# Kernel tuning notes

Hardware: AMD Instinct MI355X
Metric: run time of the kernel (lower is better)

## Reference

```python
import jax, jax.numpy as jnp
import numpy as np

B, C, H, W, P = 16, 512, 64, 64, 32


def setup_inputs() -> dict:
    key = jax.random.key(0)
    k1, k2, k3 = jax.random.split(key, 3)
    inputs = jax.random.normal(k1, (B, C, H, W), dtype=jnp.float32)
    weight = jax.random.uniform(k2, (P, C, 1, 1), dtype=jnp.float32)
    smooth_factor = jax.random.normal(k3, (P,), dtype=jnp.float32)
    return {"inputs": inputs, "weight": weight, "smooth_factor": smooth_factor}


def reference(inputs, weight, smooth_factor):
    b, c, h, w = inputs.shape
    p = weight.shape[0]
    n = h * w
    centers = weight.reshape(p, c)                      # [P,C]
    x = inputs.reshape(b, c, n)                         # [B,C,N]

    # distance-based logits: 2<c,x> - |x|^2 - |c|^2, clamped at 0
    cx = jnp.einsum('pc,bcn->bpn', centers, x)          # [B,P,N]
    x_sq = jnp.sum(x * x, axis=1, keepdims=True)        # [B,1,N]
    c_sq = jnp.sum(centers * centers, axis=1)[None, :, None]  # [1,P,1]
    beta = jax.nn.sigmoid(smooth_factor)                # [P]
    logits = jnp.minimum(2.0 * cx - x_sq - c_sq, 0.0) / beta[None, :, None]
    assign = jax.nn.softmax(logits, axis=1)             # [B,P,N]

    # assignment-weighted pooling
    qx = jnp.einsum('bpn,bcn->bpc', assign, x)          # [B,P,C]
    sum_ass = jnp.clip(jnp.sum(assign, axis=2, keepdims=True), 1e-5)  # [B,P,1]
    sigma = jnp.sqrt(beta / 2.0)                        # [P]
    out = (qx / sum_ass - centers[None, :, :]) / sigma[None, :, None]

    # L2-normalize over channel dim (torch F.normalize, eps=1e-12)
    norm = jnp.sqrt(jnp.sum(out * out, axis=2, keepdims=True))
    outputs = out / jnp.maximum(norm, 1e-12)
    outputs_t = jnp.transpose(outputs, (0, 2, 1))       # [B,C,P]
    assign_map = assign.reshape(b, p, h, w)             # [B,P,H,W]
    return outputs_t, assign_map
```

## Files before the change

### kernel.cpp

```cpp
#include <hip/hip_runtime.h>

constexpr int BB = 16;
constexpr int CC = 512;
constexpr int PP = 32;
constexpr int NN = 4096;
constexpr int TN = 128;

using f32x4 = __attribute__((ext_vector_type(4))) float;
using bf16x8 = __attribute__((ext_vector_type(8))) short;
typedef unsigned int uint;

__device__ __forceinline__ ushort f2bf(float f) {
  unsigned u = __builtin_bit_cast(unsigned, f);
  u += 0x7FFFu + ((u >> 16) & 1u);
  return (ushort)(u >> 16);
}

__device__ __forceinline__ uint packbf(float f) {
  uint u = __builtin_bit_cast(uint, f);
  uint hi = (u + (0x7FFFu + ((u >> 16) & 1u))) >> 16;
  float hif = __builtin_bit_cast(float, hi << 16);
  float lof = f - hif;
  uint ul = __builtin_bit_cast(uint, lof);
  uint lo = (ul + (0x7FFFu + ((ul >> 16) & 1u))) >> 16;
  return (lo << 16) | hi;
}

struct BfPair { bf16x8 hi, lo; };

__device__ __forceinline__ BfPair unpack8(const uint* __restrict__ row, int co) {
  uint4 a = *(const uint4*)(row + co);
  uint4 b = *(const uint4*)(row + co + 4);
  union { bf16x8 v; uint d[4]; } H, L;
  H.d[0] = (a.x & 0xffffu) | (a.y << 16); L.d[0] = (a.x >> 16) | (a.y & 0xffff0000u);
  H.d[1] = (a.z & 0xffffu) | (a.w << 16); L.d[1] = (a.z >> 16) | (a.w & 0xffff0000u);
  H.d[2] = (b.x & 0xffffu) | (b.y << 16); L.d[2] = (b.x >> 16) | (b.y & 0xffff0000u);
  H.d[3] = (b.z & 0xffffu) | (b.w << 16); L.d[3] = (b.z >> 16) | (b.w & 0xffff0000u);
  return {H.v, L.v};
}

__global__ __launch_bounds__(64) void prep_kernel(
    const float* __restrict__ w, const float* __restrict__ sf,
    float* __restrict__ beta, float* __restrict__ rbeta,
    float* __restrict__ csq) {
  int p = blockIdx.x;
  int t = threadIdx.x;
  float s = 0.f;
  for (int i = t; i < CC; i += 64) {
    float v = w[p * CC + i];
    s = fmaf(v, v, s);
  }
#pragma unroll
  for (int off = 32; off; off >>= 1) s += __shfl_down(s, off);
  if (t == 0) {
    csq[p] = s;
    float e = __expf(-sf[p]);
    rbeta[p] = 1.f + e;
    beta[p] = 1.f / (1.f + e);
  }
}

__global__ __launch_bounds__(256, 3) void fused_kernel(
    const float* __restrict__ x, const float* __restrict__ w,
    const float* __restrict__ rbeta_, const float* __restrict__ csq_,
    float* __restrict__ assign_out, float* __restrict__ sum_ass,
    float* __restrict__ qx) {
  __shared__ uint xpk[128][68];
  __shared__ uint cpk[32][68];
  __shared__ float xsqw[4][4][32];
  __shared__ float xsqf[128];
  ushort(*xt)[136] = (ushort(*)[136]) & xpk[0][0];
  ushort(*abf)[136] = (ushort(*)[136]) & cpk[0][0];

  int tid = threadIdx.x;
  int wv = tid >> 6, lane = tid & 63;
  int l15 = lane & 15, lg = lane >> 4;
  int b = blockIdx.x >> 5;
  int n0 = (blockIdx.x & 31) * TN;

  int c_s = tid >> 2;
  int q = tid & 3;
  int p_s = tid >> 3;
  int cq8 = (tid & 7) << 3;

  const float* xb = x + (size_t)b * CC * NN + n0 + q * 32;
  const float* wb = w + (size_t)p_s * CC + cq8;

  f32x4 acc[2][2];
#pragma unroll
  for (int i = 0; i < 2; ++i)
#pragma unroll
    for (int j = 0; j < 2; ++j) acc[i][j] = {0.f, 0.f, 0.f, 0.f};
  float sq[32];
#pragma unroll
  for (int i = 0; i < 32; ++i) sq[i] = 0.f;

  float4 xr[8], wr0, wr1;
#pragma unroll
  for (int i = 0; i < 8; ++i)
    xr[i] = *(const float4*)&xb[(size_t)c_s * NN + i * 4];
  wr0 = *(const float4*)&wb[0];
  wr1 = *(const float4*)&wb[4];
#pragma unroll
  for (int i = 0; i < 8; ++i) {
    float4 v = xr[i];
    sq[4 * i + 0] = fmaf(v.x, v.x, sq[4 * i + 0]);
    sq[4 * i + 1] = fmaf(v.y, v.y, sq[4 * i + 1]);
    sq[4 * i + 2] = fmaf(v.z, v.z, sq[4 * i + 2]);
    sq[4 * i + 3] = fmaf(v.w, v.w, sq[4 * i + 3]);
    int nr = q * 32 + i * 4;
    xpk[nr + 0][c_s] = packbf(v.x);
    xpk[nr + 1][c_s] = packbf(v.y);
    xpk[nr + 2][c_s] = packbf(v.z);
    xpk[nr + 3][c_s] = packbf(v.w);
  }
  {
    uint4 u0 = {packbf(wr0.x), packbf(wr0.y), packbf(wr0.z), packbf(wr0.w)};
    uint4 u1 = {packbf(wr1.x), packbf(wr1.y), packbf(wr1.z), packbf(wr1.w)};
    *(uint4*)&cpk[p_s][cq8] = u0;
    *(uint4*)&cpk[p_s][cq8 + 4] = u1;
  }
  __syncthreads();

  for (int c0 = 0; c0 < CC; c0 += 64) {
    bool more = (c0 + 64 < CC);
    if (more) {
#pragma unroll
      for (int i = 0; i < 8; ++i)
        xr[i] = *(const float4*)&xb[(size_t)(c0 + 64 + c_s) * NN + i * 4];
      wr0 = *(const float4*)&wb[c0 + 64];
      wr1 = *(const float4*)&wb[c0 + 64 + 4];
    }
#pragma unroll
    for (int ks = 0; ks < 2; ++ks) {
      int co = ks * 32 + lg * 8;
      BfPair A0 = unpack8(&cpk[l15][0], co);
      BfPair A1 = unpack8(&cpk[l15 + 16][0], co);
      BfPair B0 = unpack8(&xpk[wv * 32 + l15][0], co);
      BfPair B1 = unpack8(&xpk[wv * 32 + 16 + l15][0], co);
      acc[0][0] = __builtin_amdgcn_mfma_f32_16x16x32_bf16(A0.hi, B0.hi, acc[0][0], 0, 0, 0);
      acc[0][1] = __builtin_amdgcn_mfma_f32_16x16x32_bf16(A0.hi, B1.hi, acc[0][1], 0, 0, 0);
      acc[1][0] = __builtin_amdgcn_mfma_f32_16x16x32_bf16(A1.hi, B0.hi, acc[1][0], 0, 0, 0);
      acc[1][1] = __builtin_amdgcn_mfma_f32_16x16x32_bf16(A1.hi, B1.hi, acc[1][1], 0, 0, 0);
      acc[0][0] = __builtin_amdgcn_mfma_f32_16x16x32_bf16(A0.hi, B0.lo, acc[0][0], 0, 0, 0);
      acc[0][1] = __builtin_amdgcn_mfma_f32_16x16x32_bf16(A0.hi, B1.lo, acc[0][1], 0, 0, 0);
      acc[1][0] = __builtin_amdgcn_mfma_f32_16x16x32_bf16(A1.hi, B0.lo, acc[1][0], 0, 0, 0);
      acc[1][1] = __builtin_amdgcn_mfma_f32_16x16x32_bf16(A1.hi, B1.lo, acc[1][1], 0, 0, 0);
      acc[0][0] = __builtin_amdgcn_mfma_f32_16x16x32_bf16(A0.lo, B0.hi, acc[0][0], 0, 0, 0);
      acc[0][1] = __builtin_amdgcn_mfma_f32_16x16x32_bf16(A0.lo, B1.hi, acc[0][1], 0, 0, 0);
      acc[1][0] = __builtin_amdgcn_mfma_f32_16x16x32_bf16(A1.lo, B0.hi, acc[1][0], 0, 0, 0);
      acc[1][1] = __builtin_amdgcn_mfma_f32_16x16x32_bf16(A1.lo, B1.hi, acc[1][1], 0, 0, 0);
    }
    if (more) {
      __syncthreads();
#pragma unroll
      for (int i = 0; i < 8; ++i) {
        float4 v = xr[i];
        sq[4 * i + 0] = fmaf(v.x, v.x, sq[4 * i + 0]);
        sq[4 * i + 1] = fmaf(v.y, v.y, sq[4 * i + 1]);
        sq[4 * i + 2] = fmaf(v.z, v.z, sq[4 * i + 2]);
        sq[4 * i + 3] = fmaf(v.w, v.w, sq[4 * i + 3]);
        int nr = q * 32 + i * 4;
        xpk[nr + 0][c_s] = packbf(v.x);
        xpk[nr + 1][c_s] = packbf(v.y);
        xpk[nr + 2][c_s] = packbf(v.z);
        xpk[nr + 3][c_s] = packbf(v.w);
      }
      uint4 u0 = {packbf(wr0.x), packbf(wr0.y), packbf(wr0.z), packbf(wr0.w)};
      uint4 u1 = {packbf(wr1.x), packbf(wr1.y), packbf(wr1.z), packbf(wr1.w)};
      *(uint4*)&cpk[p_s][cq8] = u0;
      *(uint4*)&cpk[p_s][cq8 + 4] = u1;
      __syncthreads();
    }
  }

#pragma unroll
  for (int i = 0; i < 32; ++i) {
    sq[i] += __shfl_xor(sq[i], 4);
    sq[i] += __shfl_xor(sq[i], 8);
    sq[i] += __shfl_xor(sq[i], 16);
    sq[i] += __shfl_xor(sq[i], 32);
  }
  if ((lane >> 2) == 0) {
#pragma unroll
    for (int i = 0; i < 32; ++i) xsqw[wv][lane & 3][i] = sq[i];
  }
  __syncthreads();
  if (tid < 128)
    xsqf[tid] = xsqw[0][tid >> 5][tid & 31] + xsqw[1][tid >> 5][tid & 31] +
                xsqw[2][tid >> 5][tid & 31] + xsqw[3][tid >> 5][tid & 31];
  __syncthreads();

  float xsqn0 = xsqf[wv * 32 + l15];
  float xsqn1 = xsqf[wv * 32 + 16 + l15];

  float csqv[2][4], rbv[2][4];
#pragma unroll
  for (int pf = 0; pf < 2; ++pf)
#pragma unroll
    for (int i = 0; i < 4; ++i) {
      int p = pf * 16 + lg * 4 + i;
      csqv[pf][i] = csq_[p];
      rbv[pf][i] = rbeta_[p];
    }

  float L[2][2][4];
  float m0 = -3.4e38f, m1 = -3.4e38f;
#pragma unroll
  for (int pf = 0; pf < 2; ++pf)
#pragma unroll
    for (int i = 0; i < 4; ++i) {
      float l0 = fminf(2.f * acc[pf][0][i] - xsqn0 - csqv[pf][i], 0.f) * rbv[pf][i];
      float l1 = fminf(2.f * acc[pf][1][i] - xsqn1 - csqv[pf][i], 0.f) * rbv[pf][i];
      L[pf][0][i] = l0; L[pf][1][i] = l1;
      m0 = fmaxf(m0, l0); m1 = fmaxf(m1, l1);
    }
  m0 = fmaxf(m0, __shfl_xor(m0, 16)); m0 = fmaxf(m0, __shfl_xor(m0, 32));
  m1 = fmaxf(m1, __shfl_xor(m1, 16)); m1 = fmaxf(m1, __shfl_xor(m1, 32));
  float s0 = 0.f, s1 = 0.f;
#pragma unroll
  for (int pf = 0; pf < 2; ++pf)
#pragma unroll
    for (int i = 0; i < 4; ++i) {
      float e0 = __expf(L[pf][0][i] - m0);
      float e1 = __expf(L[pf][1][i] - m1);
      L[pf][0][i] = e0; L[pf][1][i] = e1;
      s0 += e0; s1 += e1;
    }
  s0 += __shfl_xor(s0, 16); s0 += __shfl_xor(s0, 32);
  s1 += __shfl_xor(s1, 16); s1 += __shfl_xor(s1, 32);
  float inv0 = 1.f / s0, inv1 = 1.f / s1;

  float* aoB = assign_out + (size_t)b * PP * NN + n0 + wv * 32 + l15;
#pragma unroll
  for (int pf = 0; pf < 2; ++pf)
#pragma unroll
    for (int i = 0; i < 4; ++i) {
      int p = pf * 16 + lg * 4 + i;
      float a0 = L[pf][0][i] * inv0;
      float a1 = L[pf][1][i] * inv1;
      aoB[(size_t)p * NN] = a0;
      aoB[(size_t)p * NN + 16] = a1;
      abf[p][wv * 32 + l15] = f2bf(a0);
      abf[p][wv * 32 + 16 + l15] = f2bf(a1);
      float v = a0 + a1;
      v += __shfl_xor(v, 1); v += __shfl_xor(v, 2);
      v += __shfl_xor(v, 4); v += __shfl_xor(v, 8);
      if (l15 == 0) atomicAdd(&sum_ass[b * PP + p], v);
    }

  int c_s2 = tid >> 1;
  int nh2 = (tid & 1) << 6;
  const float* xg = x + (size_t)b * CC * NN + n0;

  for (int ch = 0; ch < 4; ++ch) {
    __syncthreads();
#pragma unroll
    for (int h = 0; h < 2; ++h) {
      float4 v[8];
#pragma unroll
      for (int i = 0; i < 8; ++i)
        v[i] = *(const float4*)&xg[(size_t)(ch * 128 + c_s2) * NN + nh2 + h * 32 + i * 4];
#pragma unroll
      for (int i = 0; i < 8; ++i) {
        ushort4 u;
        u.x = f2bf(v[i].x); u.y = f2bf(v[i].y);
        u.z = f2bf(v[i].z); u.w = f2bf(v[i].w);
        *(ushort4*)&xt[c_s2][nh2 + h * 32 + i * 4] = u;
      }
    }
    __syncthreads();

    f32x4 q2[2][2];
#pragma unroll
    for (int pf = 0; pf < 2; ++pf)
#pragma unroll
      for (int cf = 0; cf < 2; ++cf) q2[pf][cf] = {0.f, 0.f, 0.f, 0.f};
#pragma unroll
    for (int ks = 0; ks < 4; ++ks) {
      int ko = ks * 32 + lg * 8;
      bf16x8 A0 = *(const bf16x8*)&abf[l15][ko];
      bf16x8 A1 = *(const bf16x8*)&abf[l15 + 16][ko];
#pragma unroll
      for (int cf = 0; cf < 2; ++cf) {
        bf16x8 Bv = *(const bf16x8*)&xt[wv * 32 + cf * 16 + l15][ko];
        q2[0][cf] = __builtin_amdgcn_mfma_f32_16x16x32_bf16(A0, Bv, q2[0][cf], 0, 0, 0);
        q2[1][cf] = __builtin_amdgcn_mfma_f32_16x16x32_bf16(A1, Bv, q2[1][cf], 0, 0, 0);
      }
    }
#pragma unroll
    for (int pf = 0; pf < 2; ++pf)
#pragma unroll
      for (int cf = 0; cf < 2; ++cf)
#pragma unroll
        for (int i = 0; i < 4; ++i) {
          int p = pf * 16 + lg * 4 + i;
          int c = ch * 128 + wv * 32 + cf * 16 + l15;
          atomicAdd(&qx[((size_t)b * PP + p) * CC + c], q2[pf][cf][i]);
        }
  }
}

__global__ __launch_bounds__(256) void finalize_kernel(
    const float* __restrict__ qx, const float* __restrict__ w,
    const float* __restrict__ beta, const float* __restrict__ sum_ass,
    float* __restrict__ out_t) {
  int b = blockIdx.x >> 5;
  int p = blockIdx.x & 31;
  int tid = threadIdx.x;
  int wave = tid >> 6, lane = tid & 63;

  float inv_sa = 1.f / fmaxf(sum_ass[b * PP + p], 1e-5f);
  float rsig = rsqrtf(0.5f * beta[p]);

  int c0 = tid, c1 = tid + 256;
  const float* qrow = qx + ((size_t)b * PP + p) * CC;
  const float* wrow = w + (size_t)p * CC;
  float t0 = (qrow[c0] * inv_sa - wrow[c0]) * rsig;
  float t1 = (qrow[c1] * inv_sa - wrow[c1]) * rsig;

  float nr = t0 * t0 + t1 * t1;
#pragma unroll
  for (int off = 32; off; off >>= 1) nr += __shfl_down(nr, off);
  __shared__ float red[4];
  if (lane == 0) red[wave] = nr;
  __syncthreads();
  float norm2 = red[0] + red[1] + red[2] + red[3];
  float scale = 1.f / fmaxf(sqrtf(norm2), 1e-12f);

  float* ob = out_t + (size_t)b * CC * PP + p;
  ob[(size_t)c0 * PP] = t0 * scale;
  ob[(size_t)c1 * PP] = t1 * scale;
}

extern "C" void kernel_launch(void* const* d_in, const int* in_sizes, int n_in,
                              void* d_out, int out_size, void* d_ws,
                              size_t ws_size, hipStream_t stream) {
  const float* x = (const float*)d_in[0];
  const float* w = (const float*)d_in[1];
  const float* sf = (const float*)d_in[2];

  float* out_t = (float*)d_out;
  float* assign = out_t + (size_t)BB * CC * PP;

  float* ws = (float*)d_ws;
  float* beta = ws;
  float* rbeta = ws + 32;
  float* csq = ws + 64;
  float* sum_ass = ws + 96;
  float* qx = ws + 608;

  hipMemsetAsync(sum_ass, 0, (512 + (size_t)BB * PP * CC) * sizeof(float),
                 stream);
  prep_kernel<<<PP, 64, 0, stream>>>(w, sf, beta, rbeta, csq);
  fused_kernel<<<BB * 32, 256, 0, stream>>>(x, w, rbeta, csq, assign,
                                            sum_ass, qx);
  finalize_kernel<<<BB * PP, 256, 0, stream>>>(qx, w, beta, sum_ass, out_t);
}
```

Baseline: 95.37 us.

## Halve spatial tile to double grid, split qx atomics, fold memset into prep

```diff
diff --git a/kernel.cpp b/kernel.cpp
--- a/kernel.cpp
+++ b/kernel.cpp
@@ -4,7 +4,7 @@
 constexpr int CC = 512;
 constexpr int PP = 32;
 constexpr int NN = 4096;
-constexpr int TN = 128;
+constexpr int TN = 64;
 
 using f32x4 = __attribute__((ext_vector_type(4))) float;
 using bf16x8 = __attribute__((ext_vector_type(8))) short;
@@ -42,73 +42,78 @@
 __global__ __launch_bounds__(64) void prep_kernel(
     const float* __restrict__ w, const float* __restrict__ sf,
     float* __restrict__ beta, float* __restrict__ rbeta,
-    float* __restrict__ csq) {
-  int p = blockIdx.x;
+    float* __restrict__ csq, float* __restrict__ zbuf) {
   int t = threadIdx.x;
-  float s = 0.f;
-  for (int i = t; i < CC; i += 64) {
-    float v = w[p * CC + i];
-    s = fmaf(v, v, s);
-  }
-#pragma unroll
-  for (int off = 32; off; off >>= 1) s += __shfl_down(s, off);
-  if (t == 0) {
-    csq[p] = s;
-    float e = __expf(-sf[p]);
-    rbeta[p] = 1.f + e;
-    beta[p] = 1.f / (1.f + e);
-  }
-}
-
-__global__ __launch_bounds__(256, 3) void fused_kernel(
+  float4* z4 = (float4*)zbuf;
+  for (int i = blockIdx.x * 64 + t; i < 131200; i += 256 * 64)
+    z4[i] = make_float4(0.f, 0.f, 0.f, 0.f);
+  if (blockIdx.x < PP) {
+    int p = blockIdx.x;
+    float s = 0.f;
+    for (int i = t; i < CC; i += 64) {
+      float v = w[p * CC + i];
+      s = fmaf(v, v, s);
+    }
+#pragma unroll
+    for (int off = 32; off; off >>= 1) s += __shfl_down(s, off);
+    if (t == 0) {
+      csq[p] = s;
+      float e = __expf(-sf[p]);
+      rbeta[p] = 1.f + e;
+      beta[p] = 1.f / (1.f + e);
+    }
+  }
+}
+
+__global__ __launch_bounds__(256, 4) void fused_kernel(
     const float* __restrict__ x, const float* __restrict__ w,
     const float* __restrict__ rbeta_, const float* __restrict__ csq_,
     float* __restrict__ assign_out, float* __restrict__ sum_ass,
-    float* __restrict__ qx) {
-  __shared__ uint xpk[128][68];
-  __shared__ uint cpk[32][68];
-  __shared__ float xsqw[4][4][32];
-  __shared__ float xsqf[128];
-  ushort(*xt)[136] = (ushort(*)[136]) & xpk[0][0];
-  ushort(*abf)[136] = (ushort(*)[136]) & cpk[0][0];
+    float* __restrict__ qx2) {
+  __shared__ uint shbuf[6528];
+  __shared__ ushort abf[PP][72];
+  __shared__ float xsqw[4][4][16];
+  __shared__ float xsqf[TN];
+
+  uint(*xpk)[68] = (uint(*)[68])shbuf;
+  uint(*cpk)[68] = (uint(*)[68])(shbuf + 64 * 68);
+  ushort(*xt)[72] = (ushort(*)[72])shbuf;
 
   int tid = threadIdx.x;
   int wv = tid >> 6, lane = tid & 63;
   int l15 = lane & 15, lg = lane >> 4;
-  int b = blockIdx.x >> 5;
-  int n0 = (blockIdx.x & 31) * TN;
+  int b = blockIdx.x >> 6;
+  int n0 = (blockIdx.x & 63) * TN;
 
   int c_s = tid >> 2;
-  int q = tid & 3;
+  int nw = (tid & 3) << 4;
   int p_s = tid >> 3;
   int cq8 = (tid & 7) << 3;
 
-  const float* xb = x + (size_t)b * CC * NN + n0 + q * 32;
+  const float* xb = x + (size_t)b * CC * NN + n0 + nw;
   const float* wb = w + (size_t)p_s * CC + cq8;
 
-  f32x4 acc[2][2];
-#pragma unroll
-  for (int i = 0; i < 2; ++i)
-#pragma unroll
-    for (int j = 0; j < 2; ++j) acc[i][j] = {0.f, 0.f, 0.f, 0.f};
-  float sq[32];
-#pragma unroll
-  for (int i = 0; i < 32; ++i) sq[i] = 0.f;
-
-  float4 xr[8], wr0, wr1;
-#pragma unroll
-  for (int i = 0; i < 8; ++i)
+  f32x4 acc[2];
+  acc[0] = {0.f, 0.f, 0.f, 0.f};
+  acc[1] = {0.f, 0.f, 0.f, 0.f};
+  float sq[16];
+#pragma unroll
+  for (int i = 0; i < 16; ++i) sq[i] = 0.f;
+
+  float4 xr[4], wr0, wr1;
+#pragma unroll
+  for (int i = 0; i < 4; ++i)
     xr[i] = *(const float4*)&xb[(size_t)c_s * NN + i * 4];
   wr0 = *(const float4*)&wb[0];
   wr1 = *(const float4*)&wb[4];
 #pragma unroll
-  for (int i = 0; i < 8; ++i) {
+  for (int i = 0; i < 4; ++i) {
     float4 v = xr[i];
     sq[4 * i + 0] = fmaf(v.x, v.x, sq[4 * i + 0]);
     sq[4 * i + 1] = fmaf(v.y, v.y, sq[4 * i + 1]);
     sq[4 * i + 2] = fmaf(v.z, v.z, sq[4 * i + 2]);
     sq[4 * i + 3] = fmaf(v.w, v.w, sq[4 * i + 3]);
-    int nr = q * 32 + i * 4;
+    int nr = nw + i * 4;
     xpk[nr + 0][c_s] = packbf(v.x);
     xpk[nr + 1][c_s] = packbf(v.y);
     xpk[nr + 2][c_s] = packbf(v.z);
@@ -126,7 +131,7 @@
     bool more = (c0 + 64 < CC);
     if (more) {
 #pragma unroll
-      for (int i = 0; i < 8; ++i)
+      for (int i = 0; i < 4; ++i)
         xr[i] = *(const float4*)&xb[(size_t)(c0 + 64 + c_s) * NN + i * 4];
       wr0 = *(const float4*)&wb[c0 + 64];
       wr1 = *(const float4*)&wb[c0 + 64 + 4];
@@ -136,31 +141,24 @@
       int co = ks * 32 + lg * 8;
       BfPair A0 = unpack8(&cpk[l15][0], co);
       BfPair A1 = unpack8(&cpk[l15 + 16][0], co);
-      BfPair B0 = unpack8(&xpk[wv * 32 + l15][0], co);
-      BfPair B1 = unpack8(&xpk[wv * 32 + 16 + l15][0], co);
-      acc[0][0] = __builtin_amdgcn_mfma_f32_16x16x32_bf16(A0.hi, B0.hi, acc[0][0], 0, 0, 0);
-      acc[0][1] = __builtin_amdgcn_mfma_f32_16x16x32_bf16(A0.hi, B1.hi, acc[0][1], 0, 0, 0);
-      acc[1][0] = __builtin_amdgcn_mfma_f32_16x16x32_bf16(A1.hi, B0.hi, acc[1][0], 0, 0, 0);
-      acc[1][1] = __builtin_amdgcn_mfma_f32_16x16x32_bf16(A1.hi, B1.hi, acc[1][1], 0, 0, 0);
-      acc[0][0] = __builtin_amdgcn_mfma_f32_16x16x32_bf16(A0.hi, B0.lo, acc[0][0], 0, 0, 0);
-      acc[0][1] = __builtin_amdgcn_mfma_f32_16x16x32_bf16(A0.hi, B1.lo, acc[0][1], 0, 0, 0);
-      acc[1][0] = __builtin_amdgcn_mfma_f32_16x16x32_bf16(A1.hi, B0.lo, acc[1][0], 0, 0, 0);
-      acc[1][1] = __builtin_amdgcn_mfma_f32_16x16x32_bf16(A1.hi, B1.lo, acc[1][1], 0, 0, 0);
-      acc[0][0] = __builtin_amdgcn_mfma_f32_16x16x32_bf16(A0.lo, B0.hi, acc[0][0], 0, 0, 0);
-      acc[0][1] = __builtin_amdgcn_mfma_f32_16x16x32_bf16(A0.lo, B1.hi, acc[0][1], 0, 0, 0);
-      acc[1][0] = __builtin_amdgcn_mfma_f32_16x16x32_bf16(A1.lo, B0.hi, acc[1][0], 0, 0, 0);
-      acc[1][1] = __builtin_amdgcn_mfma_f32_16x16x32_bf16(A1.lo, B1.hi, acc[1][1], 0, 0, 0);
+      BfPair B0 = unpack8(&xpk[wv * 16 + l15][0], co);
+      acc[0] = __builtin_amdgcn_mfma_f32_16x16x32_bf16(A0.hi, B0.hi, acc[0], 0, 0, 0);
+      acc[1] = __builtin_amdgcn_mfma_f32_16x16x32_bf16(A1.hi, B0.hi, acc[1], 0, 0, 0);
+      acc[0] = __builtin_amdgcn_mfma_f32_16x16x32_bf16(A0.hi, B0.lo, acc[0], 0, 0, 0);
+      acc[1] = __builtin_amdgcn_mfma_f32_16x16x32_bf16(A1.hi, B0.lo, acc[1], 0, 0, 0);
+      acc[0] = __builtin_amdgcn_mfma_f32_16x16x32_bf16(A0.lo, B0.hi, acc[0], 0, 0, 0);
+      acc[1] = __builtin_amdgcn_mfma_f32_16x16x32_bf16(A1.lo, B0.hi, acc[1], 0, 0, 0);
     }
     if (more) {
       __syncthreads();
 #pragma unroll
-      for (int i = 0; i < 8; ++i) {
+      for (int i = 0; i < 4; ++i) {
         float4 v = xr[i];
         sq[4 * i + 0] = fmaf(v.x, v.x, sq[4 * i + 0]);
         sq[4 * i + 1] = fmaf(v.y, v.y, sq[4 * i + 1]);
         sq[4 * i + 2] = fmaf(v.z, v.z, sq[4 * i + 2]);
         sq[4 * i + 3] = fmaf(v.w, v.w, sq[4 * i + 3]);
-        int nr = q * 32 + i * 4;
+        int nr = nw + i * 4;
         xpk[nr + 0][c_s] = packbf(v.x);
         xpk[nr + 1][c_s] = packbf(v.y);
         xpk[nr + 2][c_s] = packbf(v.z);
@@ -175,98 +173,84 @@
   }
 
 #pragma unroll
-  for (int i = 0; i < 32; ++i) {
+  for (int i = 0; i < 16; ++i) {
     sq[i] += __shfl_xor(sq[i], 4);
     sq[i] += __shfl_xor(sq[i], 8);
     sq[i] += __shfl_xor(sq[i], 16);
     sq[i] += __shfl_xor(sq[i], 32);
   }
-  if ((lane >> 2) == 0) {
-#pragma unroll
-    for (int i = 0; i < 32; ++i) xsqw[wv][lane & 3][i] = sq[i];
+  if (lane < 4) {
+#pragma unroll
+    for (int i = 0; i < 16; ++i) xsqw[wv][lane][i] = sq[i];
   }
   __syncthreads();
-  if (tid < 128)
-    xsqf[tid] = xsqw[0][tid >> 5][tid & 31] + xsqw[1][tid >> 5][tid & 31] +
-                xsqw[2][tid >> 5][tid & 31] + xsqw[3][tid >> 5][tid & 31];
+  if (tid < TN)
+    xsqf[tid] = xsqw[0][tid >> 4][tid & 15] + xsqw[1][tid >> 4][tid & 15] +
+                xsqw[2][tid >> 4][tid & 15] + xsqw[3][tid >> 4][tid & 15];
   __syncthreads();
 
-  float xsqn0 = xsqf[wv * 32 + l15];
-  float xsqn1 = xsqf[wv * 32 + 16 + l15];
-
-  float csqv[2][4], rbv[2][4];
+  float xsqn = xsqf[wv * 16 + l15];
+
+  float L[2][4];
+  float m = -3.4e38f;
 #pragma unroll
   for (int pf = 0; pf < 2; ++pf)
 #pragma unroll
     for (int i = 0; i < 4; ++i) {
       int p = pf * 16 + lg * 4 + i;
-      csqv[pf][i] = csq_[p];
-      rbv[pf][i] = rbeta_[p];
-    }
-
-  float L[2][2][4];
-  float m0 = -3.4e38f, m1 = -3.4e38f;
+      float l = fminf(2.f * acc[pf][i] - xsqn - csq_[p], 0.f) * rbeta_[p];
+      L[pf][i] = l;
+      m = fmaxf(m, l);
+    }
+  m = fmaxf(m, __shfl_xor(m, 16));
+  m = fmaxf(m, __shfl_xor(m, 32));
+  float s = 0.f;
 #pragma unroll
   for (int pf = 0; pf < 2; ++pf)
 #pragma unroll
     for (int i = 0; i < 4; ++i) {
-      float l0 = fminf(2.f * acc[pf][0][i] - xsqn0 - csqv[pf][i], 0.f) * rbv[pf][i];
-      float l1 = fminf(2.f * acc[pf][1][i] - xsqn1 - csqv[pf][i], 0.f) * rbv[pf][i];
-      L[pf][0][i] = l0; L[pf][1][i] = l1;
-      m0 = fmaxf(m0, l0); m1 = fmaxf(m1, l1);
-    }
-  m0 = fmaxf(m0, __shfl_xor(m0, 16)); m0 = fmaxf(m0, __shfl_xor(m0, 32));
-  m1 = fmaxf(m1, __shfl_xor(m1, 16)); m1 = fmaxf(m1, __shfl_xor(m1, 32));
-  float s0 = 0.f, s1 = 0.f;
-#pragma unroll
-  for (int pf = 0; pf < 2; ++pf)
-#pragma unroll
-    for (int i = 0; i < 4; ++i) {
-      float e0 = __expf(L[pf][0][i] - m0);
-      float e1 = __expf(L[pf][1][i] - m1);
-      L[pf][0][i] = e0; L[pf][1][i] = e1;
-      s0 += e0; s1 += e1;
-    }
-  s0 += __shfl_xor(s0, 16); s0 += __shfl_xor(s0, 32);
-  s1 += __shfl_xor(s1, 16); s1 += __shfl_xor(s1, 32);
-  float inv0 = 1.f / s0, inv1 = 1.f / s1;
-
-  float* aoB = assign_out + (size_t)b * PP * NN + n0 + wv * 32 + l15;
+      float e = __expf(L[pf][i] - m);
+      L[pf][i] = e;
+      s += e;
+    }
+  s += __shfl_xor(s, 16);
+  s += __shfl_xor(s, 32);
+  float inv = 1.f / s;
+
+  int nl = wv * 16 + l15;
+  float* aoB = assign_out + (size_t)b * PP * NN + n0 + nl;
 #pragma unroll
   for (int pf = 0; pf < 2; ++pf)
 #pragma unroll
     for (int i = 0; i < 4; ++i) {
       int p = pf * 16 + lg * 4 + i;
-      float a0 = L[pf][0][i] * inv0;
-      float a1 = L[pf][1][i] * inv1;
-      aoB[(size_t)p * NN] = a0;
-      aoB[(size_t)p * NN + 16] = a1;
-      abf[p][wv * 32 + l15] = f2bf(a0);
-      abf[p][wv * 32 + 16 + l15] = f2bf(a1);
-      float v = a0 + a1;
+      float a = L[pf][i] * inv;
+      aoB[(size_t)p * NN] = a;
+      abf[p][nl] = f2bf(a);
+      float v = a;
       v += __shfl_xor(v, 1); v += __shfl_xor(v, 2);
       v += __shfl_xor(v, 4); v += __shfl_xor(v, 8);
       if (l15 == 0) atomicAdd(&sum_ass[b * PP + p], v);
     }
 
   int c_s2 = tid >> 1;
-  int nh2 = (tid & 1) << 6;
+  int nh2 = (tid & 1) << 5;
   const float* xg = x + (size_t)b * CC * NN + n0;
+  float* qxp = qx2 + (size_t)(blockIdx.x & 1) * BB * PP * CC;
 
   for (int ch = 0; ch < 4; ++ch) {
     __syncthreads();
-#pragma unroll
-    for (int h = 0; h < 2; ++h) {
+    {
       float4 v[8];
 #pragma unroll
       for (int i = 0; i < 8; ++i)
-        v[i] = *(const float4*)&xg[(size_t)(ch * 128 + c_s2) * NN + nh2 + h * 32 + i * 4];
+        v[i] = *(const float4*)&xg[(size_t)(ch * 128 + c_s2) * NN + nh2 + i * 4];
 #pragma unroll
       for (int i = 0; i < 8; ++i) {
         ushort4 u;
         u.x = f2bf(v[i].x); u.y = f2bf(v[i].y);
         u.z = f2bf(v[i].z); u.w = f2bf(v[i].w);
-        *(ushort4*)&xt[c_s2][nh2 + h * 32 + i * 4] = u;
+        *(ushort4*)&xt[c_s2][nh2 + i * 4] = u;
       }
     }
     __syncthreads();
@@ -277,7 +261,7 @@
 #pragma unroll
       for (int cf = 0; cf < 2; ++cf) q2[pf][cf] = {0.f, 0.f, 0.f, 0.f};
 #pragma unroll
-    for (int ks = 0; ks < 4; ++ks) {
+    for (int ks = 0; ks < 2; ++ks) {
       int ko = ks * 32 + lg * 8;
       bf16x8 A0 = *(const bf16x8*)&abf[l15][ko];
       bf16x8 A1 = *(const bf16x8*)&abf[l15 + 16][ko];
@@ -296,13 +280,13 @@
         for (int i = 0; i < 4; ++i) {
           int p = pf * 16 + lg * 4 + i;
           int c = ch * 128 + wv * 32 + cf * 16 + l15;
-          atomicAdd(&qx[((size_t)b * PP + p) * CC + c], q2[pf][cf][i]);
+          atomicAdd(&qxp[((size_t)b * PP + p) * CC + c], q2[pf][cf][i]);
         }
   }
 }
 
 __global__ __launch_bounds__(256) void finalize_kernel(
-    const float* __restrict__ qx, const float* __restrict__ w,
+    const float* __restrict__ qx2, const float* __restrict__ w,
     const float* __restrict__ beta, const float* __restrict__ sum_ass,
     float* __restrict__ out_t) {
   int b = blockIdx.x >> 5;
@@ -314,10 +298,13 @@
   float rsig = rsqrtf(0.5f * beta[p]);
 
   int c0 = tid, c1 = tid + 256;
-  const float* qrow = qx + ((size_t)b * PP + p) * CC;
+  const float* r0 = qx2 + ((size_t)b * PP + p) * CC;
+  const float* r1 = r0 + (size_t)BB * PP * CC;
+  float q0 = r0[c0] + r1[c0];
+  float q1 = r0[c1] + r1[c1];
   const float* wrow = w + (size_t)p * CC;
-  float t0 = (qrow[c0] * inv_sa - wrow[c0]) * rsig;
-  float t1 = (qrow[c1] * inv_sa - wrow[c1]) * rsig;
+  float t0 = (q0 * inv_sa - wrow[c0]) * rsig;
+  float t1 = (q1 * inv_sa - wrow[c1]) * rsig;
 
   float nr = t0 * t0 + t1 * t1;
 #pragma unroll
@@ -348,12 +335,10 @@
   float* rbeta = ws + 32;
   float* csq = ws + 64;
   float* sum_ass = ws + 96;
-  float* qx = ws + 608;
-
-  hipMemsetAsync(sum_ass, 0, (512 + (size_t)BB * PP * CC) * sizeof(float),
-                 stream);
-  prep_kernel<<<PP, 64, 0, stream>>>(w, sf, beta, rbeta, csq);
-  fused_kernel<<<BB * 32, 256, 0, stream>>>(x, w, rbeta, csq, assign,
-                                            sum_ass, qx);
-  finalize_kernel<<<BB * PP, 256, 0, stream>>>(qx, w, beta, sum_ass, out_t);
-}
+  float* qx2 = ws + 608;
+
+  prep_kernel<<<256, 64, 0, stream>>>(w, sf, beta, rbeta, csq, sum_ass);
+  fused_kernel<<<BB * 64, 256, 0, stream>>>(x, w, rbeta, csq, assign,
+                                            sum_ass, qx2);
+  finalize_kernel<<<BB * PP, 256, 0, stream>>>(qx2, w, beta, sum_ass, out_t);
+}
```

After: 145.9 us. 53.0% more time.
